# Performance work log

Measured on AMD Instinct MI355X. Metric: run time of the kernel, lower is better.

Reference implementation:

```python
import jax, jax.numpy as jnp
import numpy as np

KS = 3          # deform kernel size
N = KS * KS     # sampling points per output pixel
PAD = 1         # zero padding

def conv2d(x, w, stride, padding):
    return jax.lax.conv_general_dilated(
        x, w, (stride, stride), [(padding, padding), (padding, padding)],
        dimension_numbers=('NCHW', 'OIHW', 'NCHW'))

def _gather(x_flat, qx, qy, Wp):
    # x_flat: [b, c, Hp*Wp]; qx, qy: [b, h, w, N] int32 -> [b, c, h, w, N]
    b = qx.shape[0]; c = x_flat.shape[1]
    idx = (qx * Wp + qy).reshape(b, 1, -1)
    out = jnp.take_along_axis(x_flat, jnp.broadcast_to(idx, (b, c, idx.shape[-1])), axis=2)
    return out.reshape(b, c, qx.shape[1], qx.shape[2], qx.shape[3])

def deform_conv(x, w_off, b_off, w_conv):
    # learned per-pixel offsets: [b, 2N, h, w] (first N = x-offsets, last N = y-offsets)
    offset = conv2d(x, w_off, 1, PAD) + b_off[None, :, None, None]
    b, _, h, w = offset.shape
    x_pad = jnp.pad(x, ((0, 0), (0, 0), (PAD, PAD), (PAD, PAD)))
    Hp, Wp = x_pad.shape[2], x_pad.shape[3]
    # kernel-relative offsets p_n in {-1,0,1}^2
    pn_x, pn_y = jnp.meshgrid(jnp.arange(-(KS // 2), KS // 2 + 1),
                              jnp.arange(-(KS // 2), KS // 2 + 1), indexing='ij')
    p_n = jnp.concatenate([pn_x.reshape(-1), pn_y.reshape(-1)]).reshape(1, 2 * N, 1, 1)
    # base grid p_0 (1..h, 1..w in padded coordinates)
    p0_x, p0_y = jnp.meshgrid(jnp.arange(1, h + 1), jnp.arange(1, w + 1), indexing='ij')
    p_0 = jnp.concatenate([jnp.tile(p0_x[None], (N, 1, 1)),
                           jnp.tile(p0_y[None], (N, 1, 1))])[None]  # [1, 2N, h, w]
    p = (p_0 + p_n).astype(offset.dtype) + offset                   # [b, 2N, h, w]
    p = jnp.transpose(p, (0, 2, 3, 1))                              # [b, h, w, 2N]
    px, py = p[..., :N], p[..., N:]
    q = jnp.floor(jax.lax.stop_gradient(p))
    qlt_x = jnp.clip(q[..., :N], 0, Hp - 1); qlt_y = jnp.clip(q[..., N:], 0, Wp - 1)
    qrb_x = jnp.clip(q[..., :N] + 1, 0, Hp - 1); qrb_y = jnp.clip(q[..., N:] + 1, 0, Wp - 1)
    px = jnp.clip(px, 0, Hp - 1); py = jnp.clip(py, 0, Wp - 1)
    # bilinear weights (classic DCN formulation)
    g_lt = (1 + (qlt_x - px)) * (1 + (qlt_y - py))
    g_rb = (1 - (qrb_x - px)) * (1 - (qrb_y - py))
    g_lb = (1 + (qlt_x - px)) * (1 - (qrb_y - py))
    g_rt = (1 - (qrb_x - px)) * (1 + (qlt_y - py))
    x_flat = x_pad.reshape(b, x_pad.shape[1], -1)
    qi = lambda a: a.astype(jnp.int32)
    x_lt = _gather(x_flat, qi(qlt_x), qi(qlt_y), Wp)
    x_rb = _gather(x_flat, qi(qrb_x), qi(qrb_y), Wp)
    x_lb = _gather(x_flat, qi(qlt_x), qi(qrb_y), Wp)
    x_rt = _gather(x_flat, qi(qrb_x), qi(qlt_y), Wp)
    xo = (g_lt[:, None] * x_lt + g_rb[:, None] * x_rb
          + g_lb[:, None] * x_lb + g_rt[:, None] * x_rt)  # [b, c, h, w, N]
    c = xo.shape[1]
    # unfold N -> (ks, ks) blocks: [b, c, h*ks, w*ks]
    xo = xo.reshape(b, c, h, w, KS, KS).transpose(0, 1, 2, 4, 3, 5).reshape(b, c, h * KS, w * KS)
    return conv2d(xo, w_conv, KS, 0)  # stride=ks aggregation, no bias

def reference(x, w_off, b_off, w_conv, w_fc, b_fc):
    y = jax.nn.relu(deform_conv(x, w_off, b_off, w_conv))          # [b, 8, 28, 28]
    y = jax.lax.reduce_window(y, -jnp.inf, jax.lax.max,
                              (1, 1, 2, 2), (1, 1, 2, 2), 'VALID')  # [b, 8, 14, 14]
    y = y.reshape(y.shape[0], -1)
    return y @ w_fc.T + b_fc

def setup_inputs() -> dict:
    key = jax.random.key(0)
    k1, k2, k3, k4 = jax.random.split(key, 4)
    B = 4096
    return {
        'x': jax.random.normal(k1, (B, 1, 28, 28), dtype=jnp.float32),
        'w_off': jax.random.normal(k2, (18, 1, 3, 3), dtype=jnp.float32) * 0.1,
        'b_off': jnp.zeros((18,), dtype=jnp.float32),
        'w_conv': jax.random.normal(k3, (8, 1, 3, 3), dtype=jnp.float32) * 0.3,
        'w_fc': jax.random.normal(k4, (10, 8 * 14 * 14), dtype=jnp.float32) * 0.02,
        'b_fc': jnp.zeros((10,), dtype=jnp.float32),
    }
```

## Files before the change

### kernel.cpp

```cpp
#include <hip/hip_runtime.h>


#define HH 28
#define WW 28
#define HP 30
#define WP 30
#define NPOS (HH * WW)
#define NPOOL (8 * 14 * 14)

__global__ __launch_bounds__(256) void deform_net_kernel(
    const float* __restrict__ x,
    const float* __restrict__ w_off,
    const float* __restrict__ b_off,
    const float* __restrict__ w_conv,
    const float* __restrict__ w_fc,
    const float* __restrict__ b_fc,
    float* __restrict__ out)
{
    __shared__ float xs[HP * WP];
    __shared__ float red[4][10];

    const int b   = blockIdx.x;
    const int tid = threadIdx.x;

    const float* xb = x + (size_t)b * NPOS;
    for (int i = tid; i < HP * WP; i += 256) {
        int r = i / WP, c = i % WP;
        float v = 0.f;
        if (r >= 1 && r <= HH && c >= 1 && c <= WW)
            v = xb[(r - 1) * WW + (c - 1)];
        xs[i] = v;
    }
    __syncthreads();

    float fc[10];
    #pragma unroll
    for (int c = 0; c < 10; c++) fc[c] = 0.f;

    if (tid < 196) {
        const int ph = tid / 14, pw = tid % 14;
        const int h0 = 2 * ph, w0 = 2 * pw;

        float nb[16];
        #pragma unroll
        for (int i = 0; i < 4; i++)
            #pragma unroll
            for (int j = 0; j < 4; j++)
                nb[i * 4 + j] = xs[(h0 + i) * WP + (w0 + j)];

        float acc[4][8];
        #pragma unroll
        for (int p = 0; p < 4; p++)
            #pragma unroll
            for (int o = 0; o < 8; o++) acc[p][o] = 0.f;

        #pragma unroll
        for (int k = 0; k < 9; k++) {
            const int kx = k / 3, ky = k % 3;
            #pragma unroll
            for (int p = 0; p < 4; p++) {
                const int dh = p >> 1, dw = p & 1;

                float offx = b_off[k], offy = b_off[k + 9];
                #pragma unroll
                for (int t = 0; t < 9; t++) {
                    float nv = nb[(dh + t / 3) * 4 + (dw + t % 3)];
                    offx = fmaf(w_off[k * 9 + t],        nv, offx);
                    offy = fmaf(w_off[(k + 9) * 9 + t],  nv, offy);
                }

                float p_x = (float)(h0 + dh + kx) + offx;
                float p_y = (float)(w0 + dw + ky) + offy;

                float q0x = floorf(p_x), q0y = floorf(p_y);
                float qltx = fminf(fmaxf(q0x,       0.f), 29.f);
                float qlty = fminf(fmaxf(q0y,       0.f), 29.f);
                float qrbx = fminf(fmaxf(q0x + 1.f, 0.f), 29.f);
                float qrby = fminf(fmaxf(q0y + 1.f, 0.f), 29.f);
                float px   = fminf(fmaxf(p_x,       0.f), 29.f);
                float py   = fminf(fmaxf(p_y,       0.f), 29.f);

                float gltx = 1.f + (qltx - px);
                float glty = 1.f + (qlty - py);
                float grbx = 1.f - (qrbx - px);
                float grby = 1.f - (qrby - py);

                int ilx = (int)qltx, ily = (int)qlty;
                int irx = (int)qrbx, iry = (int)qrby;

                float xlt = xs[ilx * WP + ily];
                float xrb = xs[irx * WP + iry];
                float xlb = xs[ilx * WP + iry];
                float xrt = xs[irx * WP + ily];

                float s = gltx * glty * xlt + grbx * grby * xrb
                        + gltx * grby * xlb + grbx * glty * xrt;

                #pragma unroll
                for (int o = 0; o < 8; o++)
                    acc[p][o] = fmaf(w_conv[o * 9 + k], s, acc[p][o]);
            }
        }

        #pragma unroll
        for (int o = 0; o < 8; o++) {
            float m = fmaxf(fmaxf(acc[0][o], acc[1][o]),
                            fmaxf(acc[2][o], acc[3][o]));
            m = fmaxf(m, 0.f);
            const float* wrow = w_fc + o * 196 + tid;
            #pragma unroll
            for (int c = 0; c < 10; c++)
                fc[c] = fmaf(m, wrow[c * NPOOL], fc[c]);
        }
    }

    #pragma unroll
    for (int c = 0; c < 10; c++) {
        #pragma unroll
        for (int sh = 32; sh > 0; sh >>= 1)
            fc[c] += __shfl_down(fc[c], sh, 64);
    }
    const int wave = tid >> 6, lane = tid & 63;
    if (lane == 0) {
        #pragma unroll
        for (int c = 0; c < 10; c++) red[wave][c] = fc[c];
    }
    __syncthreads();
    if (tid < 10)
        out[b * 10 + tid] = red[0][tid] + red[1][tid] + red[2][tid]
                          + red[3][tid] + b_fc[tid];
}

extern "C" void kernel_launch(void* const* d_in, const int* in_sizes, int n_in,
                              void* d_out, int out_size, void* d_ws, size_t ws_size,
                              hipStream_t stream) {
    const float* x      = (const float*)d_in[0];
    const float* w_off  = (const float*)d_in[1];
    const float* b_off  = (const float*)d_in[2];
    const float* w_conv = (const float*)d_in[3];
    const float* w_fc   = (const float*)d_in[4];
    const float* b_fc   = (const float*)d_in[5];
    float* out = (float*)d_out;

    const int B = in_sizes[0] / NPOS;
    deform_net_kernel<<<B, 256, 0, stream>>>(x, w_off, b_off, w_conv, w_fc, b_fc, out);
}
```

Measured before the change: 130.8 us.

## Pack pooled cells from multiple images per block to fill all threads

Instead of one image per 256-thread block with only 196 active threads, the kernel now assigns 256 consecutive pooled cells across image boundaries to each block, staging up to three padded images in shared memory. Per-image FC partial sums are reduced serially from shared memory and combined across blocks with atomicAdd into a zero-initialised output, and the bias is added once by the cell-0 thread. This removes idle lanes and shrinks the grid, at the cost of an extra memset, atomics and a serial reduction loop over up to 256 entries.

```diff
diff --git a/kernel.cpp b/kernel.cpp
--- a/kernel.cpp
+++ b/kernel.cpp
@@ -1,12 +1,10 @@
 #include <hip/hip_runtime.h>
 
 
-#define HH 28
-#define WW 28
-#define HP 30
 #define WP 30
-#define NPOS (HH * WW)
-#define NPOOL (8 * 14 * 14)
+#define NPOS 784
+#define NPOOL 1568
+#define CELLS 196
 
 __global__ __launch_bounds__(256) void deform_net_kernel(
     const float* __restrict__ x,
@@ -15,30 +13,41 @@
     const float* __restrict__ w_conv,
     const float* __restrict__ w_fc,
     const float* __restrict__ b_fc,
-    float* __restrict__ out)
+    float* __restrict__ out,
+    int B)
 {
-    __shared__ float xs[HP * WP];
-    __shared__ float red[4][10];
+    __shared__ float xs[3][900];
+    __shared__ float fc_s[256][10];
 
-    const int b   = blockIdx.x;
-    const int tid = threadIdx.x;
+    const int tid      = threadIdx.x;
+    const int cell0    = blockIdx.x << 8;
+    const int img_base = cell0 / CELLS;
 
-    const float* xb = x + (size_t)b * NPOS;
-    for (int i = tid; i < HP * WP; i += 256) {
-        int r = i / WP, c = i % WP;
+    for (int i = tid; i < 2700; i += 256) {
+        int s = i / 900;
+        int j = i - s * 900;
+        int img = img_base + s;
         float v = 0.f;
-        if (r >= 1 && r <= HH && c >= 1 && c <= WW)
-            v = xb[(r - 1) * WW + (c - 1)];
-        xs[i] = v;
+        if (img < B) {
+            int r = j / WP, c = j - r * WP;
+            if (r >= 1 && r <= 28 && c >= 1 && c <= 28)
+                v = x[(size_t)img * NPOS + (r - 1) * 28 + (c - 1)];
+        }
+        xs[s][j] = v;
     }
     __syncthreads();
 
+    const int cg = cell0 + tid;
     float fc[10];
     #pragma unroll
     for (int c = 0; c < 10; c++) fc[c] = 0.f;
 
-    if (tid < 196) {
-        const int ph = tid / 14, pw = tid % 14;
+    if (cg < B * CELLS) {
+        const int img  = cg / CELLS;
+        const int cell = cg - img * CELLS;
+        const int slot = img - img_base;
+        const float* __restrict__ xsp = xs[slot];
+        const int ph = cell / 14, pw = cell - ph * 14;
         const int h0 = 2 * ph, w0 = 2 * pw;
 
         float nb[16];
@@ -46,7 +55,14 @@
         for (int i = 0; i < 4; i++)
             #pragma unroll
             for (int j = 0; j < 4; j++)
-                nb[i * 4 + j] = xs[(h0 + i) * WP + (w0 + j)];
+                nb[i * 4 + j] = xsp[(h0 + i) * WP + (w0 + j)];
+
+        float hbf[4], wbf[4];
+        #pragma unroll
+        for (int i = 0; i < 4; i++) {
+            hbf[i] = (float)(h0 + i);
+            wbf[i] = (float)(w0 + i);
+        }
 
         float acc[4][8];
         #pragma unroll
@@ -65,12 +81,12 @@
                 #pragma unroll
                 for (int t = 0; t < 9; t++) {
                     float nv = nb[(dh + t / 3) * 4 + (dw + t % 3)];
-                    offx = fmaf(w_off[k * 9 + t],        nv, offx);
-                    offy = fmaf(w_off[(k + 9) * 9 + t],  nv, offy);
+                    offx = fmaf(w_off[k * 9 + t],       nv, offx);
+                    offy = fmaf(w_off[(k + 9) * 9 + t], nv, offy);
                 }
 
-                float p_x = (float)(h0 + dh + kx) + offx;
-                float p_y = (float)(w0 + dw + ky) + offy;
+                float p_x = hbf[dh + kx] + offx;
+                float p_y = wbf[dw + ky] + offy;
 
                 float q0x = floorf(p_x), q0y = floorf(p_y);
                 float qltx = fminf(fmaxf(q0x,       0.f), 29.f);
@@ -87,14 +103,11 @@
 
                 int ilx = (int)qltx, ily = (int)qlty;
                 int irx = (int)qrbx, iry = (int)qrby;
+                const float* row_l = xsp + ilx * WP;
+                const float* row_r = xsp + irx * WP;
 
-                float xlt = xs[ilx * WP + ily];
-                float xrb = xs[irx * WP + iry];
-                float xlb = xs[ilx * WP + iry];
-                float xrt = xs[irx * WP + ily];
-
-                float s = gltx * glty * xlt + grbx * grby * xrb
-                        + gltx * grby * xlb + grbx * glty * xrt;
+                float s = gltx * (glty * row_l[ily] + grby * row_l[iry])
+                        + grbx * (glty * row_r[ily] + grby * row_r[iry]);
 
                 #pragma unroll
                 for (int o = 0; o < 8; o++)
@@ -102,33 +115,44 @@
             }
         }
 
+        float m[8];
         #pragma unroll
-        for (int o = 0; o < 8; o++) {
-            float m = fmaxf(fmaxf(acc[0][o], acc[1][o]),
-                            fmaxf(acc[2][o], acc[3][o]));
-            m = fmaxf(m, 0.f);
-            const float* wrow = w_fc + o * 196 + tid;
+        for (int o = 0; o < 8; o++)
+            m[o] = fmaxf(fmaxf(fmaxf(acc[0][o], acc[1][o]),
+                               fmaxf(acc[2][o], acc[3][o])), 0.f);
+
+        const float* wbase = w_fc + cell;
+        #pragma unroll
+        for (int c = 0; c < 10; c++) {
+            const float* wr = wbase + c * NPOOL;
             #pragma unroll
-            for (int c = 0; c < 10; c++)
-                fc[c] = fmaf(m, wrow[c * NPOOL], fc[c]);
+            for (int o = 0; o < 8; o++)
+                fc[c] = fmaf(m[o], wr[o * CELLS], fc[c]);
+        }
+        if (cell == 0) {
+            #pragma unroll
+            for (int c = 0; c < 10; c++) fc[c] += b_fc[c];
         }
     }
 
     #pragma unroll
-    for (int c = 0; c < 10; c++) {
-        #pragma unroll
-        for (int sh = 32; sh > 0; sh >>= 1)
-            fc[c] += __shfl_down(fc[c], sh, 64);
+    for (int c = 0; c < 10; c++) fc_s[tid][c] = fc[c];
+    __syncthreads();
+
+    if (tid < 30) {
+        int s = tid / 10, c = tid - s * 10;
+        int img = img_base + s;
+        if (img < B) {
+            int lo = img * CELLS - cell0;       if (lo < 0)   lo = 0;
+            int hi = (img + 1) * CELLS - cell0; if (hi > 256) hi = 256;
+            int lim = B * CELLS - cell0;        if (hi > lim) hi = lim;
+            if (lo < hi) {
+                float a = 0.f;
+                for (int t = lo; t < hi; t++) a += fc_s[t][c];
+                atomicAdd(&out[img * 10 + c], a);
+            }
+        }
     }
-    const int wave = tid >> 6, lane = tid & 63;
-    if (lane == 0) {
-        #pragma unroll
-        for (int c = 0; c < 10; c++) red[wave][c] = fc[c];
-    }
-    __syncthreads();
-    if (tid < 10)
-        out[b * 10 + tid] = red[0][tid] + red[1][tid] + red[2][tid]
-                          + red[3][tid] + b_fc[tid];
 }
 
 extern "C" void kernel_launch(void* const* d_in, const int* in_sizes, int n_in,
@@ -143,5 +167,10 @@
     float* out = (float*)d_out;
 
     const int B = in_sizes[0] / NPOS;
-    deform_net_kernel<<<B, 256, 0, stream>>>(x, w_off, b_off, w_conv, w_fc, b_fc, out);
+    const int ncells = B * CELLS;
+    const int grid = (ncells + 255) / 256;
+
+    hipMemsetAsync(d_out, 0, (size_t)out_size * sizeof(float), stream);
+    deform_net_kernel<<<grid, 256, 0, stream>>>(x, w_off, b_off, w_conv,
+                                                w_fc, b_fc, out, B);
 }
```

Result: slower. 163.6 us (+25.0%).
